# Optimization experiments

Measured on AMD Instinct MI355X. Metric: run time of the kernel, lower is better.

Reference implementation:

```python
import jax, jax.numpy as jnp
import numpy as np

D_MODEL = 1024
DEPTH = 1024

def setup_inputs() -> dict:
    key = jax.random.key(0)
    ks = jax.random.split(key, 7)
    scale = 1.0 / np.sqrt(D_MODEL)
    x = jax.random.normal(ks[0], (4, 2048, D_MODEL), dtype=jnp.float32)
    Wq = jax.random.normal(ks[1], (D_MODEL, DEPTH), dtype=jnp.float32) * scale
    Wk = jax.random.normal(ks[2], (D_MODEL, DEPTH), dtype=jnp.float32) * scale
    Wv = jax.random.normal(ks[3], (D_MODEL, DEPTH), dtype=jnp.float32) * scale
    bq = jnp.zeros((DEPTH,), dtype=jnp.float32)
    bk = jnp.zeros((DEPTH,), dtype=jnp.float32)
    bv = jnp.zeros((DEPTH,), dtype=jnp.float32)
    return {"x": x, "Wq": Wq, "bq": bq, "Wk": Wk, "bk": bk, "Wv": Wv, "bv": bv}

def reference(x, Wq, bq, Wk, bk, Wv, bv):
    # Q/K/V linear projections (Keras Dense: x @ W + b)
    q = jnp.einsum('bsd,de->bse', x, Wq) + bq  # [B,S,depth]
    k = jnp.einsum('bsd,de->bse', x, Wk) + bk
    v = jnp.einsum('bsd,de->bse', x, Wv) + bv
    d_k = jnp.asarray(q.shape[-1], dtype=q.dtype)
    scores = jnp.einsum('bse,bte->bst', q, k) / jnp.sqrt(d_k)  # [B,S,S]
    attn = jax.nn.softmax(scores, axis=-1)
    return jnp.einsum('bst,bte->bse', attn, v)  # [B,S,depth]
```

## Files before the change

### kernel.cpp

```cpp
#include <hip/hip_runtime.h>
#include <stdint.h>
#include <type_traits>

typedef unsigned short u16;
using short8  = __attribute__((ext_vector_type(8))) short;
using floatx4 = __attribute__((ext_vector_type(4))) float;

#define IC(n) (std::integral_constant<int, (n)>())

__device__ __forceinline__ u16 f2bf(float f) {
    unsigned u = __float_as_uint(f);
    u += 0x7fff + ((u >> 16) & 1);
    return (u16)(u >> 16);
}
__device__ __forceinline__ float bf2f(u16 h) {
    return __uint_as_float(((unsigned)h) << 16);
}

__device__ __forceinline__ void gload_lds16(const void* g, void* l) {
    auto gp = reinterpret_cast<const __attribute__((address_space(1))) unsigned int*>(
        reinterpret_cast<uintptr_t>(g));
    auto lp = reinterpret_cast<__attribute__((address_space(3))) unsigned int*>(
        reinterpret_cast<uintptr_t>(l));
    __builtin_amdgcn_global_load_lds(gp, lp, 16, 0, 0);
}

__global__ __launch_bounds__(256) void cvt_f32_bf16_kernel(
        const float* __restrict__ in, u16* __restrict__ out) {
    long i = ((long)blockIdx.x * 256 + threadIdx.x) * 4;
    float4 v = *(const float4*)(in + i);
    ushort4 o;
    o.x = f2bf(v.x); o.y = f2bf(v.y); o.z = f2bf(v.z); o.w = f2bf(v.w);
    *(ushort4*)(out + i) = o;
}

__global__ __launch_bounds__(256) void wt_kernel(
        const float* __restrict__ W0, const float* __restrict__ W1, const float* __restrict__ W2,
        u16* __restrict__ O0, u16* __restrict__ O1, u16* __restrict__ O2) {
    const float* W = blockIdx.z == 0 ? W0 : blockIdx.z == 1 ? W1 : W2;
    u16* O = blockIdx.z == 0 ? O0 : blockIdx.z == 1 ? O1 : O2;
    __shared__ float t[32][33];
    const int cx = threadIdx.x & 31, ry = threadIdx.x >> 5;
    const int d0 = blockIdx.x * 32, e0 = blockIdx.y * 32;
#pragma unroll
    for (int i = 0; i < 4; i++) t[ry + i * 8][cx] = W[(long)(d0 + ry + i * 8) * 1024 + e0 + cx];
    __syncthreads();
#pragma unroll
    for (int i = 0; i < 4; i++) O[(long)(e0 + ry + i * 8) * 1024 + d0 + cx] = f2bf(t[cx][ry + i * 8]);
}

__global__ __launch_bounds__(256) void vt_kernel(
        const u16* __restrict__ V, u16* __restrict__ Vt) {
    const int b = blockIdx.z;
    const u16* v = V + (long)b * 2048 * 1024;
    u16* o = Vt + (long)b * 1024 * 2048;
    __shared__ u16 t[32][33];
    const int cx = threadIdx.x & 31, ry = threadIdx.x >> 5;
    const int e0 = blockIdx.x * 32, t0 = blockIdx.y * 32;
#pragma unroll
    for (int i = 0; i < 4; i++) t[ry + i * 8][cx] = v[(long)(t0 + ry + i * 8) * 1024 + e0 + cx];
    __syncthreads();
#pragma unroll
    for (int i = 0; i < 4; i++) o[(long)(e0 + ry + i * 8) * 2048 + t0 + cx] = t[cx][ry + i * 8];
}

template <int MODE>
__global__ __launch_bounds__(512) void gemm8_kernel(
        const u16* __restrict__ A, const u16* __restrict__ Bt,
        void* __restrict__ out0, void* __restrict__ out1, void* __restrict__ out2,
        const float* __restrict__ b0, const float* __restrict__ b1, const float* __restrict__ b2,
        int K, int N, long sAb, long sBb, long sCb, float scale)
{
    extern __shared__ u16 lds[];
    const int tid = threadIdx.x, lane = tid & 63, wid = tid >> 6;
    const int wm = wid >> 2, wn = wid & 3;
    const int l15 = lane & 15, hib = (lane >> 4) * 16;

    const int nbx = gridDim.x;
    const int nwg = nbx * gridDim.y;
    int lin = blockIdx.y * nbx + blockIdx.x;
    lin = (lin & 7) * (nwg >> 3) + (lin >> 3);
    const long m0 = (long)(lin / nbx) * 256;
    const long n0 = (long)(lin % nbx) * 256;

    const u16* Ab = A + (long)blockIdx.z * sAb;
    const u16* Bb = Bt + (long)blockIdx.z * sBb;
    const long ldk = K;
    const int NT = K >> 6;

    auto stA = [&](int dbuf, int S, int kt) {
#pragma unroll
        for (int i = 0; i < 2; ++i) {
            const int rl = tid >> 3;
            const int R  = S * 64 + rl;
            const int cb = (tid & 7) * 16;
            const int scb = cb ^ ((R & 7) << 4);
            const u16* src = Ab + (m0 + i * 128 + R) * ldk + (long)kt * 64 + (scb >> 1);
            u16* dst = lds + dbuf * 32768 + i * 8192 + S * 4096 + wid * 512;
            gload_lds16(src, dst);
        }
    };
    auto stB = [&](int dbuf, int NHs, int kt) {
#pragma unroll
        for (int i = 0; i < 2; ++i) {
            const int c = i * 2 + (wid >> 2);
            const int h = c >> 1, rb = (c & 1) * 64;
            const int w = (wid & 3) * 64 + lane;
            const int r32 = w >> 3;
            const int R = rb + NHs * 32 + r32;
            const int cb = (w & 7) * 16;
            const int scb = cb ^ ((R & 7) << 4);
            const u16* src = Bb + (n0 + h * 128 + R) * ldk + (long)kt * 64 + (scb >> 1);
            u16* dst = lds + dbuf * 32768 + 16384 + h * 8192 + (rb + NHs * 32) * 64 + (wid & 3) * 512;
            gload_lds16(src, dst);
        }
    };

    floatx4 acc[8][4] = {};
    short8 afr[4][2], bfr[2][2];

    auto LA = [&](int dbuf, auto MHc) {
        constexpr int MH = decltype(MHc)::value;
        const char* reg = (const char*)(lds + dbuf * 32768 + wm * 8192);
#pragma unroll
        for (int fm = 0; fm < 4; ++fm)
#pragma unroll
            for (int ks = 0; ks < 2; ++ks) {
                const int r = MH * 64 + fm * 16 + l15;
                const int cb = ks * 64 + hib;
                afr[fm][ks] = *(const short8*)(reg + r * 128 + (cb ^ ((r & 7) << 4)));
            }
    };
    auto LB = [&](int dbuf, auto NHc) {
        constexpr int NH = decltype(NHc)::value;
        const char* reg = (const char*)(lds + dbuf * 32768 + 16384 + (wn >> 1) * 8192);
#pragma unroll
        for (int fn = 0; fn < 2; ++fn)
#pragma unroll
            for (int ks = 0; ks < 2; ++ks) {
                const int r = (wn & 1) * 64 + NH * 32 + fn * 16 + l15;
                const int cb = ks * 64 + hib;
                bfr[fn][ks] = *(const short8*)(reg + r * 128 + (cb ^ ((r & 7) << 4)));
            }
    };
    auto MM = [&](auto MHc, auto NHc) {
        constexpr int MH = decltype(MHc)::value;
        constexpr int NH = decltype(NHc)::value;
        __builtin_amdgcn_s_setprio(1);
#pragma unroll
        for (int fm = 0; fm < 4; ++fm)
#pragma unroll
            for (int fn = 0; fn < 2; ++fn)
#pragma unroll
                for (int ks = 0; ks < 2; ++ks)
                    acc[MH * 4 + fm][NH * 2 + fn] = __builtin_amdgcn_mfma_f32_16x16x32_bf16(
                        afr[fm][ks], bfr[fn][ks], acc[MH * 4 + fm][NH * 2 + fn], 0, 0, 0);
        __builtin_amdgcn_s_setprio(0);
    };

#define BAR()   __builtin_amdgcn_s_barrier()
#define WAIT0() asm volatile("s_waitcnt lgkmcnt(0)" ::: "memory")

    stA(0, 0, 0); stA(0, 1, 0); stB(0, 0, 0); stB(0, 1, 0);
    stA(1, 0, 1); stB(1, 1, 1); stA(1, 1, 1);
    asm volatile("s_waitcnt vmcnt(6)");
    BAR();

    auto pair = [&](auto LASTC, int kt0) {
        constexpr bool L = decltype(LASTC)::value;
        LA(0, IC(0)); LB(0, IC(0));
        stB(1, 0, kt0 + 1);
        asm volatile("s_waitcnt lgkmcnt(8)");
        BAR(); WAIT0(); MM(IC(0), IC(0)); BAR();
        LB(0, IC(1));
        if (!L) stA(0, 0, kt0 + 2);
        BAR(); WAIT0(); MM(IC(0), IC(1)); BAR();
        LA(0, IC(1));
        if (!L) stB(0, 1, kt0 + 2);
        BAR(); WAIT0(); MM(IC(1), IC(1)); BAR();
        LB(0, IC(0));
        if (!L) stA(0, 1, kt0 + 2);
        BAR(); WAIT0(); MM(IC(1), IC(0));
        if (L) asm volatile("s_waitcnt vmcnt(0)");
        else   asm volatile("s_waitcnt vmcnt(6)");
        BAR();
        LA(1, IC(0)); LB(1, IC(0));
        if (!L) stB(0, 0, kt0 + 2);
        asm volatile("s_waitcnt lgkmcnt(8)");
        BAR(); WAIT0(); MM(IC(0), IC(0)); BAR();
        LB(1, IC(1));
        if (!L) stA(1, 0, kt0 + 3);
        BAR(); WAIT0(); MM(IC(0), IC(1)); BAR();
        LA(1, IC(1));
        if (!L) stB(1, 1, kt0 + 3);
        BAR(); WAIT0(); MM(IC(1), IC(1)); BAR();
        LB(1, IC(0));
        if (!L) stA(1, 1, kt0 + 3);
        BAR(); WAIT0(); MM(IC(1), IC(0));
        if (L) asm volatile("s_waitcnt vmcnt(0)");
        else   asm volatile("s_waitcnt vmcnt(6)");
        BAR();
    };

    const int NITER = NT >> 1;
    int it = 0;
    for (; it < NITER - 1; ++it) pair(std::false_type{}, 2 * it);
    pair(std::true_type{}, 2 * it);

#undef BAR
#undef WAIT0

    const int cr = (lane >> 4) * 4, cc = l15;
    if (MODE == 0) {
        const int sel = (int)(n0 >> 10);
        u16* O = (u16*)(sel == 0 ? out0 : sel == 1 ? out1 : out2);
        const float* bias = sel == 0 ? b0 : sel == 1 ? b1 : b2;
        const long nc0 = n0 & 1023;
#pragma unroll
        for (int an = 0; an < 4; ++an) {
            const long col = nc0 + wn * 64 + an * 16 + cc;
            const float bvv = bias[col];
#pragma unroll
            for (int am = 0; am < 8; ++am) {
                const long row = m0 + wm * 128 + am * 16 + cr;
#pragma unroll
                for (int j = 0; j < 4; ++j)
                    O[(row + j) * 1024 + col] = f2bf(acc[am][an][j] + bvv);
            }
        }
    } else {
#pragma unroll
        for (int an = 0; an < 4; ++an) {
            const long col = n0 + wn * 64 + an * 16 + cc;
#pragma unroll
            for (int am = 0; am < 8; ++am) {
                const long row = m0 + wm * 128 + am * 16 + cr;
#pragma unroll
                for (int j = 0; j < 4; ++j) {
                    const long idx = (long)blockIdx.z * sCb + (row + j) * (long)N + col;
                    if (MODE == 1) ((u16*)out0)[idx] = f2bf(acc[am][an][j] * scale);
                    else           ((float*)out0)[idx] = acc[am][an][j];
                }
            }
        }
    }
}

__global__ __launch_bounds__(256) void softmax_kernel(u16* __restrict__ S) {
    u16* p = S + (long)blockIdx.x * 2048;
    const int tid = threadIdx.x;
    union { int4 q; u16 u[8]; } in;
    in.q = *(const int4*)(p + tid * 8);
    float v[8];
#pragma unroll
    for (int i = 0; i < 8; i++) v[i] = bf2f(in.u[i]);
    float mx = v[0];
#pragma unroll
    for (int i = 1; i < 8; i++) mx = fmaxf(mx, v[i]);
#pragma unroll
    for (int off = 32; off; off >>= 1) mx = fmaxf(mx, __shfl_xor(mx, off));
    __shared__ float red[8];
    if ((tid & 63) == 0) red[tid >> 6] = mx;
    __syncthreads();
    mx = fmaxf(fmaxf(red[0], red[1]), fmaxf(red[2], red[3]));
    float s = 0.f;
#pragma unroll
    for (int i = 0; i < 8; i++) { v[i] = __expf(v[i] - mx); s += v[i]; }
#pragma unroll
    for (int off = 32; off; off >>= 1) s += __shfl_xor(s, off);
    if ((tid & 63) == 0) red[4 + (tid >> 6)] = s;
    __syncthreads();
    s = red[4] + red[5] + red[6] + red[7];
    const float inv = 1.f / s;
    union { int4 q; u16 u[8]; } out;
#pragma unroll
    for (int i = 0; i < 8; i++) out.u[i] = f2bf(v[i] * inv);
    *(int4*)(p + tid * 8) = out.q;
}

extern "C" void kernel_launch(void* const* d_in, const int* in_sizes, int n_in,
                              void* d_out, int out_size, void* d_ws, size_t ws_size,
                              hipStream_t stream) {
    const float* x  = (const float*)d_in[0];
    const float* Wq = (const float*)d_in[1];
    const float* bq = (const float*)d_in[2];
    const float* Wk = (const float*)d_in[3];
    const float* bk = (const float*)d_in[4];
    const float* Wv = (const float*)d_in[5];
    const float* bv = (const float*)d_in[6];
    float* out = (float*)d_out;

    char* ws = (char*)d_ws;
    const long MB = 1L << 20;
    u16* xb = (u16*)(ws);
    u16* wt = (u16*)(ws + 16 * MB);
    u16* Q  = (u16*)(ws + 22 * MB);
    u16* Kb = (u16*)(ws + 38 * MB);
    u16* Vb = (u16*)(ws + 54 * MB);
    u16* Vt = (u16*)(ws + 70 * MB);
    u16* Sc = (u16*)(ws + 86 * MB);

    (void)hipFuncSetAttribute((const void*)gemm8_kernel<0>, hipFuncAttributeMaxDynamicSharedMemorySize, 131072);
    (void)hipFuncSetAttribute((const void*)gemm8_kernel<1>, hipFuncAttributeMaxDynamicSharedMemorySize, 131072);
    (void)hipFuncSetAttribute((const void*)gemm8_kernel<2>, hipFuncAttributeMaxDynamicSharedMemorySize, 131072);

    cvt_f32_bf16_kernel<<<8192, 256, 0, stream>>>(x, xb);
    wt_kernel<<<dim3(32, 32, 3), 256, 0, stream>>>(Wq, Wk, Wv, wt, wt + 1024 * 1024, wt + 2 * 1024 * 1024);
    gemm8_kernel<0><<<dim3(12, 32, 1), 512, 131072, stream>>>(
        xb, wt, Q, Kb, Vb, bq, bk, bv, 1024, 3072, 0, 0, 0, 1.f);
    vt_kernel<<<dim3(32, 64, 4), 256, 0, stream>>>(Vb, Vt);
    gemm8_kernel<1><<<dim3(8, 8, 4), 512, 131072, stream>>>(
        Q, Kb, Sc, nullptr, nullptr, nullptr, nullptr, nullptr,
        1024, 2048, 2048L * 1024, 2048L * 1024, 2048L * 2048, 0.03125f);
    softmax_kernel<<<8192, 256, 0, stream>>>(Sc);
    gemm8_kernel<2><<<dim3(4, 8, 4), 512, 131072, stream>>>(
        Sc, Vt, out, nullptr, nullptr, nullptr, nullptr, nullptr,
        2048, 1024, 2048L * 2048, 1024L * 2048, 2048L * 1024, 1.f);
}
```

Baseline: 198.6 us.

## Fuse V transpose into projection epilogue and double-buffer MFMA fragment registers

The QKV projection epilogue now writes V directly in transposed [b, e, t] layout with ushort4 stores, so the separate V-transpose kernel and its extra buffer round trip are removed. The GEMM main loop now loads A and B fragments into two register sets (A/B halves) up front and drops the explicit lgkmcnt waits, leaving the compiler to insert LDS waits. It also adds a min-blocks hint of 2 to launch_bounds. The larger fragment register footprint and the occupancy hint may cause spills or register pressure. The transposed stores are 8-byte strided writes instead of coalesced rows.

Result: slower. 294.2 us (+48.1%).

```diff
diff --git a/kernel.cpp b/kernel.cpp
--- a/kernel.cpp
+++ b/kernel.cpp
@@ -5,8 +5,6 @@
 typedef unsigned short u16;
 using short8  = __attribute__((ext_vector_type(8))) short;
 using floatx4 = __attribute__((ext_vector_type(4))) float;
-
-#define IC(n) (std::integral_constant<int, (n)>())
 
 __device__ __forceinline__ u16 f2bf(float f) {
     unsigned u = __float_as_uint(f);
@@ -49,23 +47,8 @@
     for (int i = 0; i < 4; i++) O[(long)(e0 + ry + i * 8) * 1024 + d0 + cx] = f2bf(t[cx][ry + i * 8]);
 }
 
-__global__ __launch_bounds__(256) void vt_kernel(
-        const u16* __restrict__ V, u16* __restrict__ Vt) {
-    const int b = blockIdx.z;
-    const u16* v = V + (long)b * 2048 * 1024;
-    u16* o = Vt + (long)b * 1024 * 2048;
-    __shared__ u16 t[32][33];
-    const int cx = threadIdx.x & 31, ry = threadIdx.x >> 5;
-    const int e0 = blockIdx.x * 32, t0 = blockIdx.y * 32;
-#pragma unroll
-    for (int i = 0; i < 4; i++) t[ry + i * 8][cx] = v[(long)(t0 + ry + i * 8) * 1024 + e0 + cx];
-    __syncthreads();
-#pragma unroll
-    for (int i = 0; i < 4; i++) o[(long)(e0 + ry + i * 8) * 2048 + t0 + cx] = t[cx][ry + i * 8];
-}
-
 template <int MODE>
-__global__ __launch_bounds__(512) void gemm8_kernel(
+__global__ __launch_bounds__(512, 2) void gemm8_kernel(
         const u16* __restrict__ A, const u16* __restrict__ Bt,
         void* __restrict__ out0, void* __restrict__ out1, void* __restrict__ out2,
         const float* __restrict__ b0, const float* __restrict__ b1, const float* __restrict__ b2,
@@ -117,10 +100,10 @@
     };
 
     floatx4 acc[8][4] = {};
-    short8 afr[4][2], bfr[2][2];
-
-    auto LA = [&](int dbuf, auto MHc) {
-        constexpr int MH = decltype(MHc)::value;
+    short8 afrA[4][2], afrB[4][2];
+    short8 bfrA[2][2], bfrB[2][2];
+
+    auto LA = [&](int dbuf, int MH, short8 (&dst)[4][2]) {
         const char* reg = (const char*)(lds + dbuf * 32768 + wm * 8192);
 #pragma unroll
         for (int fm = 0; fm < 4; ++fm)
@@ -128,11 +111,10 @@
             for (int ks = 0; ks < 2; ++ks) {
                 const int r = MH * 64 + fm * 16 + l15;
                 const int cb = ks * 64 + hib;
-                afr[fm][ks] = *(const short8*)(reg + r * 128 + (cb ^ ((r & 7) << 4)));
-            }
-    };
-    auto LB = [&](int dbuf, auto NHc) {
-        constexpr int NH = decltype(NHc)::value;
+                dst[fm][ks] = *(const short8*)(reg + r * 128 + (cb ^ ((r & 7) << 4)));
+            }
+    };
+    auto LB = [&](int dbuf, int NH, short8 (&dst)[2][2]) {
         const char* reg = (const char*)(lds + dbuf * 32768 + 16384 + (wn >> 1) * 8192);
 #pragma unroll
         for (int fn = 0; fn < 2; ++fn)
@@ -140,12 +122,10 @@
             for (int ks = 0; ks < 2; ++ks) {
                 const int r = (wn & 1) * 64 + NH * 32 + fn * 16 + l15;
                 const int cb = ks * 64 + hib;
-                bfr[fn][ks] = *(const short8*)(reg + r * 128 + (cb ^ ((r & 7) << 4)));
-            }
-    };
-    auto MM = [&](auto MHc, auto NHc) {
-        constexpr int MH = decltype(MHc)::value;
-        constexpr int NH = decltype(NHc)::value;
+                dst[fn][ks] = *(const short8*)(reg + r * 128 + (cb ^ ((r & 7) << 4)));
+            }
+    };
+    auto MM = [&](short8 (&a)[4][2], short8 (&b)[2][2], int MH, int NH) {
         __builtin_amdgcn_s_setprio(1);
 #pragma unroll
         for (int fm = 0; fm < 4; ++fm)
@@ -154,12 +134,11 @@
 #pragma unroll
                 for (int ks = 0; ks < 2; ++ks)
                     acc[MH * 4 + fm][NH * 2 + fn] = __builtin_amdgcn_mfma_f32_16x16x32_bf16(
-                        afr[fm][ks], bfr[fn][ks], acc[MH * 4 + fm][NH * 2 + fn], 0, 0, 0);
+                        a[fm][ks], b[fn][ks], acc[MH * 4 + fm][NH * 2 + fn], 0, 0, 0);
         __builtin_amdgcn_s_setprio(0);
     };
 
-#define BAR()   __builtin_amdgcn_s_barrier()
-#define WAIT0() asm volatile("s_waitcnt lgkmcnt(0)" ::: "memory")
+#define BAR() __builtin_amdgcn_s_barrier()
 
     stA(0, 0, 0); stA(0, 1, 0); stB(0, 0, 0); stB(0, 1, 0);
     stA(1, 0, 1); stB(1, 1, 1); stA(1, 1, 1);
@@ -168,35 +147,29 @@
 
     auto pair = [&](auto LASTC, int kt0) {
         constexpr bool L = decltype(LASTC)::value;
-        LA(0, IC(0)); LB(0, IC(0));
+        LA(0, 0, afrA); LB(0, 0, bfrA); LB(0, 1, bfrB);
         stB(1, 0, kt0 + 1);
-        asm volatile("s_waitcnt lgkmcnt(8)");
-        BAR(); WAIT0(); MM(IC(0), IC(0)); BAR();
-        LB(0, IC(1));
+        BAR(); MM(afrA, bfrA, 0, 0); BAR();
+        LA(0, 1, afrB);
         if (!L) stA(0, 0, kt0 + 2);
-        BAR(); WAIT0(); MM(IC(0), IC(1)); BAR();
-        LA(0, IC(1));
+        BAR(); MM(afrA, bfrB, 0, 1); BAR();
         if (!L) stB(0, 1, kt0 + 2);
-        BAR(); WAIT0(); MM(IC(1), IC(1)); BAR();
-        LB(0, IC(0));
+        BAR(); MM(afrB, bfrB, 1, 1); BAR();
         if (!L) stA(0, 1, kt0 + 2);
-        BAR(); WAIT0(); MM(IC(1), IC(0));
+        BAR(); MM(afrB, bfrA, 1, 0);
         if (L) asm volatile("s_waitcnt vmcnt(0)");
         else   asm volatile("s_waitcnt vmcnt(6)");
         BAR();
-        LA(1, IC(0)); LB(1, IC(0));
+        LA(1, 0, afrA); LB(1, 0, bfrA); LB(1, 1, bfrB);
         if (!L) stB(0, 0, kt0 + 2);
-        asm volatile("s_waitcnt lgkmcnt(8)");
-        BAR(); WAIT0(); MM(IC(0), IC(0)); BAR();
-        LB(1, IC(1));
+        BAR(); MM(afrA, bfrA, 0, 0); BAR();
+        LA(1, 1, afrB);
         if (!L) stA(1, 0, kt0 + 3);
-        BAR(); WAIT0(); MM(IC(0), IC(1)); BAR();
-        LA(1, IC(1));
+        BAR(); MM(afrA, bfrB, 0, 1); BAR();
         if (!L) stB(1, 1, kt0 + 3);
-        BAR(); WAIT0(); MM(IC(1), IC(1)); BAR();
-        LB(1, IC(0));
+        BAR(); MM(afrB, bfrB, 1, 1); BAR();
         if (!L) stA(1, 1, kt0 + 3);
-        BAR(); WAIT0(); MM(IC(1), IC(0));
+        BAR(); MM(afrB, bfrA, 1, 0);
         if (L) asm volatile("s_waitcnt vmcnt(0)");
         else   asm volatile("s_waitcnt vmcnt(6)");
         BAR();
@@ -208,24 +181,45 @@
     pair(std::true_type{}, 2 * it);
 
 #undef BAR
-#undef WAIT0
 
     const int cr = (lane >> 4) * 4, cc = l15;
     if (MODE == 0) {
         const int sel = (int)(n0 >> 10);
-        u16* O = (u16*)(sel == 0 ? out0 : sel == 1 ? out1 : out2);
-        const float* bias = sel == 0 ? b0 : sel == 1 ? b1 : b2;
         const long nc0 = n0 & 1023;
-#pragma unroll
-        for (int an = 0; an < 4; ++an) {
-            const long col = nc0 + wn * 64 + an * 16 + cc;
-            const float bvv = bias[col];
-#pragma unroll
-            for (int am = 0; am < 8; ++am) {
-                const long row = m0 + wm * 128 + am * 16 + cr;
-#pragma unroll
-                for (int j = 0; j < 4; ++j)
-                    O[(row + j) * 1024 + col] = f2bf(acc[am][an][j] + bvv);
+        if (sel < 2) {
+            u16* O = (u16*)(sel == 0 ? out0 : out1);
+            const float* bias = sel == 0 ? b0 : b1;
+#pragma unroll
+            for (int an = 0; an < 4; ++an) {
+                const long col = nc0 + wn * 64 + an * 16 + cc;
+                const float bvv = bias[col];
+#pragma unroll
+                for (int am = 0; am < 8; ++am) {
+                    const long row = m0 + wm * 128 + am * 16 + cr;
+#pragma unroll
+                    for (int j = 0; j < 4; ++j)
+                        O[(row + j) * 1024 + col] = f2bf(acc[am][an][j] + bvv);
+                }
+            }
+        } else {
+            u16* O = (u16*)out2;
+            const long b = m0 >> 11;
+            const long tb = (m0 & 2047) + wm * 128;
+#pragma unroll
+            for (int an = 0; an < 4; ++an) {
+                const long e = nc0 + wn * 64 + an * 16 + cc;
+                const float bvv = b2[e];
+                u16* Oe = O + b * 1024 * 2048 + e * 2048;
+#pragma unroll
+                for (int am = 0; am < 8; ++am) {
+                    const long t = tb + am * 16 + cr;
+                    ushort4 w;
+                    w.x = f2bf(acc[am][an][0] + bvv);
+                    w.y = f2bf(acc[am][an][1] + bvv);
+                    w.z = f2bf(acc[am][an][2] + bvv);
+                    w.w = f2bf(acc[am][an][3] + bvv);
+                    *(ushort4*)(Oe + t) = w;
+                }
             }
         }
     } else {
@@ -296,9 +290,8 @@
     u16* wt = (u16*)(ws + 16 * MB);
     u16* Q  = (u16*)(ws + 22 * MB);
     u16* Kb = (u16*)(ws + 38 * MB);
-    u16* Vb = (u16*)(ws + 54 * MB);
-    u16* Vt = (u16*)(ws + 70 * MB);
-    u16* Sc = (u16*)(ws + 86 * MB);
+    u16* Vt = (u16*)(ws + 54 * MB);
+    u16* Sc = (u16*)(ws + 70 * MB);
 
     (void)hipFuncSetAttribute((const void*)gemm8_kernel<0>, hipFuncAttributeMaxDynamicSharedMemorySize, 131072);
     (void)hipFuncSetAttribute((const void*)gemm8_kernel<1>, hipFuncAttributeMaxDynamicSharedMemorySize, 131072);
@@ -307,8 +300,7 @@
     cvt_f32_bf16_kernel<<<8192, 256, 0, stream>>>(x, xb);
     wt_kernel<<<dim3(32, 32, 3), 256, 0, stream>>>(Wq, Wk, Wv, wt, wt + 1024 * 1024, wt + 2 * 1024 * 1024);
     gemm8_kernel<0><<<dim3(12, 32, 1), 512, 131072, stream>>>(
-        xb, wt, Q, Kb, Vb, bq, bk, bv, 1024, 3072, 0, 0, 0, 1.f);
-    vt_kernel<<<dim3(32, 64, 4), 256, 0, stream>>>(Vb, Vt);
+        xb, wt, Q, Kb, Vt, bq, bk, bv, 1024, 3072, 0, 0, 0, 1.f);
     gemm8_kernel<1><<<dim3(8, 8, 4), 512, 131072, stream>>>(
         Q, Kb, Sc, nullptr, nullptr, nullptr, nullptr, nullptr,
         1024, 2048, 2048L * 1024, 2048L * 1024, 2048L * 2048, 0.03125f);
```
